# Optimization experiments

Measured on AMD Instinct MI355X. Metric: run time of the kernel, lower is better.

The kernel has to match this reference:

```python
import jax, jax.numpy as jnp
import numpy as np
from jax import lax

H = 256          # hidden_size
VOCAB = 30000
N_OPS = 9
N_COLS = 16
T = 4            # num_time_steps
Q = 64           # question length
N_NUM = 8        # numbers appearing in the question
ROWS = 1_000_000

# operation indices (Neural Programmer, ICLR 2016 op set)
OP_SUM, OP_COUNT, OP_DIFF, OP_GREATER, OP_LESSER, OP_AND, OP_OR, OP_ASSIGN, OP_RESET = range(N_OPS)


def setup_inputs() -> dict:
    key = jax.random.key(0)
    ks = jax.random.split(key, 13)
    s = 0.05
    f32 = jnp.float32
    return {
        "input_question": jax.random.randint(ks[0], (Q,), 0, VOCAB),
        "input_question_numbers": jax.random.randint(ks[1], (N_NUM,), 0, 100),
        "left_word_indices": jax.random.randint(ks[2], (N_NUM,), 0, Q),
        "table": jax.random.normal(ks[3], (ROWS, N_COLS), f32),
        # learned parameters
        "emb": jax.random.normal(ks[4], (VOCAB, H), f32) * s,      # question word embeddings
        "Wx": jax.random.normal(ks[5], (H, H), f32) * s,           # question RNN input weight
        "Wh": jax.random.normal(ks[6], (H, H), f32) * s,           # question RNN recurrent weight
        "W_op": jax.random.normal(ks[7], (H, 2 * H), f32) * s,     # selector (op branch)
        "op_emb": jax.random.normal(ks[8], (N_OPS, H), f32) * s,   # operation embeddings
        "W_col": jax.random.normal(ks[9], (H, 2 * H), f32) * s,    # selector (column branch)
        "col_emb": jax.random.normal(ks[10], (N_COLS, H), f32) * s,# column embeddings
        "W_hist": jax.random.normal(ks[11], (H, 3 * H), f32) * s,  # history RNN
        "U": jax.random.normal(ks[12], (2, H), f32) * s,           # lesser/greater pivot vectors
    }


def reference(input_question, input_question_numbers, left_word_indices, table,
              emb, Wx, Wh, W_op, op_emb, W_col, col_emb, W_hist, U):
    dt = table.dtype
    hid = Wx.shape[0]

    # ---- question RNN (simple tanh RNN) ----
    xs = emb[input_question]                               # [Q, H]
    def step(h, x):
        h2 = jnp.tanh(x @ Wx.T + h @ Wh.T)
        return h2, h2
    q, hs = lax.scan(step, jnp.zeros((hid,), dt), xs)      # q=[H], hs=[Q,H]

    # ---- pivot computation (z_matrix = hidden states left of each number) ----
    z = hs[left_word_indices]                              # [N_NUM, H]
    nums = input_question_numbers.astype(dt)               # [N_NUM]
    l_pivot = jax.nn.softmax(z @ U[0]) @ nums              # scalar
    g_pivot = jax.nn.softmax(z @ U[1]) @ nums              # scalar

    # soft comparison maps (pivots are timestep-independent; compute once)
    sel_l = jax.nn.sigmoid(l_pivot - table)                # [R, C] ~ [table < l_pivot]
    sel_g = jax.nn.sigmoid(table - g_pivot)                # [R, C] ~ [table > g_pivot]

    h_hist = jnp.zeros((hid,), dt)
    scalars = [jnp.zeros((), dt)]
    rs_list = [jnp.ones((table.shape[0],), dt)]
    lookup = jnp.zeros(table.shape, dt)

    for _ in range(T):
        rs1 = rs_list[-1]
        rs2 = rs_list[max(0, len(rs_list) - 2)]
        s1 = scalars[-1]
        s3 = scalars[max(0, len(scalars) - 3)]

        # selector: soft op / column distributions from [question; history]
        qh = jnp.concatenate([q, h_hist])                  # [2H]
        a_op = jax.nn.softmax(op_emb @ jnp.tanh(W_op @ qh))    # [N_OPS]
        a_col = jax.nn.softmax(col_emb @ jnp.tanh(W_col @ qh)) # [N_COLS]

        # row select (soft mixture over ops)
        rs = (a_op[OP_GREATER] * (sel_g @ a_col)
              + a_op[OP_LESSER] * (sel_l @ a_col)
              + a_op[OP_AND] * jnp.minimum(rs1, rs2)
              + a_op[OP_OR] * jnp.maximum(rs1, rs2)
              + a_op[OP_RESET] * jnp.ones_like(rs1)
              + (a_op[OP_SUM] + a_op[OP_COUNT] + a_op[OP_DIFF] + a_op[OP_ASSIGN]) * rs1)

        # scalar answer
        scalar = (a_op[OP_SUM] * jnp.sum(rs1 @ table)
                  + a_op[OP_COUNT] * jnp.sum(rs1)
                  + a_op[OP_DIFF] * (s3 - s1))

        # lookup answer: assign op prints selected rows/columns
        lookup = a_op[OP_ASSIGN] * rs[:, None] * a_col[None, :]

        # history RNN
        c = jnp.concatenate([a_op @ op_emb, a_col @ col_emb, h_hist])  # [3H]
        h_hist = jnp.tanh(W_hist @ c)

        rs_list.append(rs)
        scalars.append(scalar)

    return scalars[-1], lookup
```

## Files before the change

### kernel.cpp

```cpp
#include <hip/hip_runtime.h>
#include <hip/hip_fp16.h>
#include <math.h>

#define HDIM   256
#define QLEN   64
#define NNUM   8
#define NOPS   9
#define NCOLS  16
#define TSTEPS 4


#define WS_LPIV 0
#define WS_GPIV 1
#define WS_ACOL 2
#define WS_AOP  66
#define WS_Q    112
#define WS_PQO  368
#define WS_PQC  624
#define WS_HS   880
#define WS_XP   2928
#define WS_AH   19312
#define WS_BH   21616
#define WS_WH16 25712
#define WS_M16  42096
#define WS_PART 140400
#define NBLK_C  2048

typedef _Float16 f16x8 __attribute__((ext_vector_type(8)));
typedef _Float16 f16x4 __attribute__((ext_vector_type(4)));
typedef float    f32x4 __attribute__((ext_vector_type(4)));

__device__ __forceinline__ float fast_tanh(float x) {
    return 1.0f - 2.0f / (__expf(2.0f * x) + 1.0f);
}

__global__ void precompute_kernel(const int* __restrict__ q,
                                  const float* __restrict__ emb,
                                  const float* __restrict__ Wx,
                                  const float* __restrict__ Wh,
                                  const float* __restrict__ W_op,
                                  const float* __restrict__ W_col,
                                  const float* __restrict__ W_hist,
                                  const float* __restrict__ op_emb,
                                  const float* __restrict__ col_emb,
                                  float* __restrict__ ws) {
    int gid = blockIdx.x * 256 + threadIdx.x;
    if (gid < QLEN * HDIM) {
        int t = gid >> 8, j = gid & 255;
        const float4* x4 = (const float4*)(emb + (size_t)q[t] * HDIM);
        const float4* w4 = (const float4*)(Wx + (size_t)j * HDIM);
        float s = 0.f;
        for (int k = 0; k < HDIM / 4; k++) {
            float4 a = x4[k], b = w4[k];
            s += a.x * b.x + a.y * b.y + a.z * b.z + a.w * b.w;
        }
        ws[WS_XP + t * HDIM + j] = s;
    } else if (gid < QLEN * HDIM + HDIM * NOPS) {
        int idx = gid - QLEN * HDIM;
        int j = idx / NOPS, o = idx % NOPS;
        const float4* w4 = (const float4*)(W_hist + (size_t)j * (3 * HDIM));
        const float4* e4 = (const float4*)(op_emb + (size_t)o * HDIM);
        float s = 0.f;
        for (int k = 0; k < HDIM / 4; k++) {
            float4 a = w4[k], b = e4[k];
            s += a.x * b.x + a.y * b.y + a.z * b.z + a.w * b.w;
        }
        ws[WS_AH + idx] = s;
    } else if (gid < QLEN * HDIM + HDIM * NOPS + HDIM * NCOLS) {
        int idx = gid - QLEN * HDIM - HDIM * NOPS;
        int j = idx / NCOLS, c = idx % NCOLS;
        const float4* w4 = (const float4*)(W_hist + (size_t)j * (3 * HDIM) + HDIM);
        const float4* e4 = (const float4*)(col_emb + (size_t)c * HDIM);
        float s = 0.f;
        for (int k = 0; k < HDIM / 4; k++) {
            float4 a = w4[k], b = e4[k];
            s += a.x * b.x + a.y * b.y + a.z * b.z + a.w * b.w;
        }
        ws[WS_BH + idx] = s;
    } else if (gid < 22784 + 16384) {
        int did = gid - 22784;
        int hidx = did * 2;
        int e = hidx & 7, qr = (hidx >> 3) & 15, quad = (hidx >> 7) & 3;
        int kk = (hidx >> 9) & 7, w = hidx >> 12;
        const float* src = Wh + (size_t)(16 * w + qr) * HDIM + kk * 32 + quad * 8 + e;
        float2 v = *(const float2*)src;
        ((__half2*)(ws + WS_WH16))[did] = __floats2half2_rn(v.x, v.y);
    } else if (gid < 22784 + 16384 + 98304) {
        int did = gid - (22784 + 16384);
        int mat = did >> 15;
        int hidx = (did & 32767) * 2;
        int e = hidx & 7, j = (hidx >> 3) & 255, i = hidx >> 11;
        const float* src;
        if (mat == 0)      src = W_op   + (size_t)j * (2 * HDIM) + HDIM     + i * 8 + e;
        else if (mat == 1) src = W_col  + (size_t)j * (2 * HDIM) + HDIM     + i * 8 + e;
        else               src = W_hist + (size_t)j * (3 * HDIM) + 2 * HDIM + i * 8 + e;
        float2 v = *(const float2*)src;
        ((__half2*)(ws + WS_M16))[did] = __floats2half2_rn(v.x, v.y);
    }
}

__global__ __launch_bounds__(256, 1) void rnn_kernel(
        float* __restrict__ ws,
        const int* __restrict__ lwi) {
    __shared__ float xpL[QLEN * HDIM];
    __shared__ _Float16 hF[2][HDIM];
    __shared__ float preact[HDIM];
    __shared__ float hsL[NNUM * HDIM];
    __shared__ float hQ[HDIM];
    __shared__ unsigned stepmask[QLEN];

    const int tid = threadIdx.x;
    const int wave = tid >> 6, lane = tid & 63;
    const int quad = lane >> 4, qr = lane & 15;

    #pragma unroll
    for (int i = 0; i < 16; i++) {
        int idx = (i * 256 + tid) * 4;
        *(float4*)(xpL + idx) = *(const float4*)(ws + WS_XP + idx);
    }
    if (tid < QLEN) {
        unsigned m = 0;
        #pragma unroll
        for (int i = 0; i < NNUM; i++) m |= (lwi[i] == tid) ? (1u << i) : 0u;
        stepmask[tid] = m;
    }
    const _Float16* wsh = (const _Float16*)(ws + WS_WH16);
    f16x8 aW[4][8];
    #pragma unroll
    for (int r = 0; r < 4; r++)
        #pragma unroll
        for (int kk = 0; kk < 8; kk++)
            aW[r][kk] = *(const f16x8*)(wsh + ((size_t)(((4 * wave + r) * 8 + kk) * 64 + lane)) * 8);
    hF[0][tid] = (_Float16)0.f;
    __syncthreads();

    for (int s = 0; s < QLEN; s++) {
        #pragma unroll
        for (int r = 0; r < 4; r++)
            #pragma unroll
            for (int kk = 0; kk < 8; kk++) {
                f32x4 t = __builtin_bit_cast(f32x4, aW[r][kk]);
                asm volatile("" : "+v"(t));
                aW[r][kk] = __builtin_bit_cast(f16x8, t);
            }

        const _Float16* hb = hF[s & 1];
        f16x8 bfrag[8];
        #pragma unroll
        for (int kk = 0; kk < 8; kk++)
            bfrag[kk] = *(const f16x8*)(hb + kk * 32 + quad * 8);
        f32x4 acc[4];
        #pragma unroll
        for (int r = 0; r < 4; r++) acc[r] = (f32x4){0.f, 0.f, 0.f, 0.f};
        #pragma unroll
        for (int kk = 0; kk < 8; kk++)
            #pragma unroll
            for (int r = 0; r < 4; r++)
                acc[r] = __builtin_amdgcn_mfma_f32_16x16x32_f16(aW[r][kk], bfrag[kk], acc[r], 0, 0, 0);
        if (qr == 0) {
            #pragma unroll
            for (int r = 0; r < 4; r++) {
                int rb = 64 * wave + 16 * r + quad * 4;
                *(f32x4*)(preact + rb) = acc[r];
            }
        }
        __syncthreads();
        {
            float h = fast_tanh(preact[tid] + xpL[s * HDIM + tid]);
            hF[(s + 1) & 1][tid] = (_Float16)h;
            unsigned m = stepmask[s];
            while (m) {
                int i = __builtin_ctz(m);
                hsL[i * HDIM + tid] = h;
                m &= m - 1;
            }
            if (s == QLEN - 1) hQ[tid] = h;
        }
        __syncthreads();
    }
    #pragma unroll
    for (int i = 0; i < NNUM; i++) ws[WS_HS + i * HDIM + tid] = hsL[i * HDIM + tid];
    ws[WS_Q + tid] = hQ[tid];
}

__global__ void qproj_kernel(const float* __restrict__ W_op,
                             const float* __restrict__ W_col,
                             float* __restrict__ ws) {
    int gid = blockIdx.x * 256 + threadIdx.x;
    int dot = gid >> 5, l = gid & 31;
    int mat = dot >> 8, j = dot & 255;
    const float* w = (mat ? W_col : W_op) + (size_t)j * (2 * HDIM) + l * 8;
    const float* qv = ws + WS_Q + l * 8;
    float4 a0 = *(const float4*)w,        a1 = *(const float4*)(w + 4);
    float4 b0 = *(const float4*)qv,       b1 = *(const float4*)(qv + 4);
    float s = a0.x * b0.x + a0.y * b0.y + a0.z * b0.z + a0.w * b0.w
            + a1.x * b1.x + a1.y * b1.y + a1.z * b1.z + a1.w * b1.w;
    s += __shfl_xor(s, 1); s += __shfl_xor(s, 2); s += __shfl_xor(s, 4);
    s += __shfl_xor(s, 8); s += __shfl_xor(s, 16);
    if (l == 0) ws[(mat ? WS_PQC : WS_PQO) + j] = s;
}

__global__ __launch_bounds__(256) void select_kernel(
        float* __restrict__ ws,
        const float* __restrict__ U,
        const int* __restrict__ nums,
        const float* __restrict__ op_emb,
        const float* __restrict__ col_emb) {
    __shared__ float zu[16];
    __shared__ float hH[HDIM];
    __shared__ float top_op[HDIM], top_col[HDIM], mh[HDIM];
    __shared__ float logits[32];
    __shared__ float aop_s[NOPS], acol_s[NCOLS];

    const int tid = threadIdx.x;

    {
        int g = tid >> 4, l = tid & 15;
        int i = g >> 1, u = g & 1;
        const float* z = ws + WS_HS + i * HDIM + l * 16;
        const float* uu = U + u * HDIM + l * 16;
        float s = 0.f;
        #pragma unroll
        for (int k = 0; k < 4; k++) {
            float4 a = *(const float4*)(z + k * 4), b = *(const float4*)(uu + k * 4);
            s += a.x * b.x + a.y * b.y + a.z * b.z + a.w * b.w;
        }
        s += __shfl_xor(s, 1); s += __shfl_xor(s, 2);
        s += __shfl_xor(s, 4); s += __shfl_xor(s, 8);
        if (l == 0) zu[g] = s;
    }
    if (tid < HDIM) hH[tid] = 0.f;
    __syncthreads();
    if (tid == 0) {
        #pragma unroll
        for (int u = 0; u < 2; u++) {
            float mx = -1e30f;
            for (int i = 0; i < NNUM; i++) mx = fmaxf(mx, zu[i * 2 + u]);
            float se = 0.f, pv = 0.f;
            for (int i = 0; i < NNUM; i++) {
                float e = __expf(zu[i * 2 + u] - mx);
                se += e;
                pv += e * (float)nums[i];
            }
            ws[u] = pv / se;
        }
    }
    __syncthreads();

    const _Float16* wsm = (const _Float16*)(ws + WS_M16);
    const float pqo = ws[WS_PQO + tid];
    const float pqc = ws[WS_PQC + tid];

    for (int t = 0; t < TSTEPS; t++) {
        float so = 0.f, sc = 0.f, sh = 0.f;
        #pragma unroll
        for (int i = 0; i < 32; i++) {
            float4 h0 = *(const float4*)(hH + i * 8);
            float4 h1 = *(const float4*)(hH + i * 8 + 4);
            f16x8 a = *(const f16x8*)(wsm + ((size_t)(0 * 32 + i) * 256 + tid) * 8);
            f16x8 b = *(const f16x8*)(wsm + ((size_t)(1 * 32 + i) * 256 + tid) * 8);
            f16x8 c = *(const f16x8*)(wsm + ((size_t)(2 * 32 + i) * 256 + tid) * 8);
            so += (float)a[0]*h0.x + (float)a[1]*h0.y + (float)a[2]*h0.z + (float)a[3]*h0.w
                + (float)a[4]*h1.x + (float)a[5]*h1.y + (float)a[6]*h1.z + (float)a[7]*h1.w;
            sc += (float)b[0]*h0.x + (float)b[1]*h0.y + (float)b[2]*h0.z + (float)b[3]*h0.w
                + (float)b[4]*h1.x + (float)b[5]*h1.y + (float)b[6]*h1.z + (float)b[7]*h1.w;
            sh += (float)c[0]*h0.x + (float)c[1]*h0.y + (float)c[2]*h0.z + (float)c[3]*h0.w
                + (float)c[4]*h1.x + (float)c[5]*h1.y + (float)c[6]*h1.z + (float)c[7]*h1.w;
        }
        top_op[tid]  = fast_tanh(pqo + so);
        top_col[tid] = fast_tanh(pqc + sc);
        mh[tid] = sh;
        __syncthreads();

        #pragma unroll
        for (int d0 = 0; d0 < 32; d0 += 8) {
            int d = d0 + (tid >> 5), l = tid & 31;
            if (d < 25) {
                float s = 0.f;
                if (d < NOPS) {
                    const float* e = op_emb + (size_t)d * HDIM;
                    #pragma unroll
                    for (int m = 0; m < 8; m++) s += e[l * 8 + m] * top_op[l * 8 + m];
                } else {
                    const float* e = col_emb + (size_t)(d - NOPS) * HDIM;
                    #pragma unroll
                    for (int m = 0; m < 8; m++) s += e[l * 8 + m] * top_col[l * 8 + m];
                }
                s += __shfl_xor(s, 1); s += __shfl_xor(s, 2); s += __shfl_xor(s, 4);
                s += __shfl_xor(s, 8); s += __shfl_xor(s, 16);
                if (l == 0) logits[d] = s;
            }
        }
        __syncthreads();
        if (tid == 0) {
            float mx = -1e30f;
            for (int o = 0; o < NOPS; o++) mx = fmaxf(mx, logits[o]);
            float se = 0.f, e[NOPS];
            for (int o = 0; o < NOPS; o++) { e[o] = __expf(logits[o] - mx); se += e[o]; }
            for (int o = 0; o < NOPS; o++) {
                float a = e[o] / se;
                aop_s[o] = a;
                ws[WS_AOP + t * NOPS + o] = a;
            }
        } else if (tid == 32) {
            float mx = -1e30f;
            for (int c = 0; c < NCOLS; c++) mx = fmaxf(mx, logits[NOPS + c]);
            float se = 0.f, e[NCOLS];
            for (int c = 0; c < NCOLS; c++) { e[c] = __expf(logits[NOPS + c] - mx); se += e[c]; }
            for (int c = 0; c < NCOLS; c++) {
                float a = e[c] / se;
                acol_s[c] = a;
                ws[WS_ACOL + t * NCOLS + c] = a;
            }
        }
        __syncthreads();
        {
            float s = mh[tid];
            const float* ah = ws + WS_AH + tid * NOPS;
            #pragma unroll
            for (int o = 0; o < NOPS; o++) s += ah[o] * aop_s[o];
            const float* bh = ws + WS_BH + tid * NCOLS;
            #pragma unroll
            for (int c = 0; c < NCOLS; c++) s += bh[c] * acol_s[c];
            float hv = fast_tanh(s);
            __syncthreads();
            hH[tid] = hv;
        }
        __syncthreads();
    }
}

__global__ __launch_bounds__(256) void table_kernel(
        const float* __restrict__ table,
        const float* __restrict__ wsc,
        float* __restrict__ wspart,
        float* __restrict__ out,
        int rows) {
    const int tid = threadIdx.x;
    const int cq = tid & 3;
    const float lpiv = wsc[WS_LPIV];
    const float gpiv = wsc[WS_GPIV];
    float4 acol4[TSTEPS];
    float wg[TSTEPS], wl[TSTEPS], wand[TSTEPS], wor[TSTEPS], wrst[TSTEPS], wpass[TSTEPS];
    #pragma unroll
    for (int t = 0; t < TSTEPS; t++) {
        acol4[t] = make_float4(wsc[WS_ACOL + t * NCOLS + cq * 4 + 0],
                               wsc[WS_ACOL + t * NCOLS + cq * 4 + 1],
                               wsc[WS_ACOL + t * NCOLS + cq * 4 + 2],
                               wsc[WS_ACOL + t * NCOLS + cq * 4 + 3]);
        wg[t]   = wsc[WS_AOP + t * NOPS + 3];
        wl[t]   = wsc[WS_AOP + t * NOPS + 4];
        wand[t] = wsc[WS_AOP + t * NOPS + 5];
        wor[t]  = wsc[WS_AOP + t * NOPS + 6];
        wrst[t] = wsc[WS_AOP + t * NOPS + 8];
        wpass[t] = wsc[WS_AOP + t * NOPS + 0] + wsc[WS_AOP + t * NOPS + 1]
                 + wsc[WS_AOP + t * NOPS + 2] + wsc[WS_AOP + t * NOPS + 7];
    }
    const float wassign = wsc[WS_AOP + 3 * NOPS + 7];

    float dAcc[TSTEPS] = {0.f, 0.f, 0.f, 0.f};
    float nAcc[TSTEPS] = {0.f, 0.f, 0.f, 0.f};
    const long rowsL = rows;

    for (long r0 = (long)blockIdx.x * 64; r0 < rowsL; r0 += (long)NBLK_C * 64) {
        long row = r0 + (tid >> 2);
        bool valid = row < rowsL;
        f32x4 tv = {0.f, 0.f, 0.f, 0.f};
        if (valid)
            tv = __builtin_nontemporal_load((const f32x4*)(table + row * NCOLS + cq * 4));
        float prs = tv.x + tv.y + tv.z + tv.w;
        float pg[4], pl[4];
        {
            float c0 = tv.x, c1 = tv.y, c2 = tv.z, c3 = tv.w;
            float sg0 = __builtin_amdgcn_rcpf(1.f + __expf(gpiv - c0));
            float sg1 = __builtin_amdgcn_rcpf(1.f + __expf(gpiv - c1));
            float sg2 = __builtin_amdgcn_rcpf(1.f + __expf(gpiv - c2));
            float sg3 = __builtin_amdgcn_rcpf(1.f + __expf(gpiv - c3));
            float sl0 = __builtin_amdgcn_rcpf(1.f + __expf(c0 - lpiv));
            float sl1 = __builtin_amdgcn_rcpf(1.f + __expf(c1 - lpiv));
            float sl2 = __builtin_amdgcn_rcpf(1.f + __expf(c2 - lpiv));
            float sl3 = __builtin_amdgcn_rcpf(1.f + __expf(c3 - lpiv));
            #pragma unroll
            for (int t = 0; t < TSTEPS; t++) {
                pg[t] = sg0 * acol4[t].x + sg1 * acol4[t].y + sg2 * acol4[t].z + sg3 * acol4[t].w;
                pl[t] = sl0 * acol4[t].x + sl1 * acol4[t].y + sl2 * acol4[t].z + sl3 * acol4[t].w;
            }
        }
        prs += __shfl_xor(prs, 1); prs += __shfl_xor(prs, 2);
        #pragma unroll
        for (int t = 0; t < TSTEPS; t++) {
            pg[t] += __shfl_xor(pg[t], 1); pg[t] += __shfl_xor(pg[t], 2);
            pl[t] += __shfl_xor(pl[t], 1); pl[t] += __shfl_xor(pl[t], 2);
        }
        float rs1 = 1.f, rs2 = 1.f;
        float vf = valid ? 1.f : 0.f;
        #pragma unroll
        for (int i = 0; i < TSTEPS; i++) {
            dAcc[i] += vf * rs1 * prs;
            nAcc[i] += vf * rs1;
            float nrs = wg[i] * pg[i] + wl[i] * pl[i]
                      + wand[i] * fminf(rs1, rs2) + wor[i] * fmaxf(rs1, rs2)
                      + wrst[i] + wpass[i] * rs1;
            rs2 = rs1;
            rs1 = nrs;
        }
        if (valid) {
            float wa = wassign * rs1;
            float* ob = out + 1 + row * NCOLS + cq * 4;
            __builtin_nontemporal_store(wa * acol4[3].x, ob + 0);
            __builtin_nontemporal_store(wa * acol4[3].y, ob + 1);
            __builtin_nontemporal_store(wa * acol4[3].z, ob + 2);
            __builtin_nontemporal_store(wa * acol4[3].w, ob + 3);
        }
    }

    #pragma unroll
    for (int i = 0; i < TSTEPS; i++) {
        #pragma unroll
        for (int off = 32; off >= 1; off >>= 1) {
            dAcc[i] += __shfl_xor(dAcc[i], off);
            nAcc[i] += __shfl_xor(nAcc[i], off);
        }
    }
    __shared__ float redl[4][8];
    int wv = tid >> 6, ln = tid & 63;
    if (ln == 0) {
        #pragma unroll
        for (int i = 0; i < TSTEPS; i++) {
            redl[wv][i] = dAcc[i];
            redl[wv][4 + i] = nAcc[i];
        }
    }
    __syncthreads();
    if (tid < 8) {
        float s = redl[0][tid] + redl[1][tid] + redl[2][tid] + redl[3][tid];
        wspart[blockIdx.x * 8 + tid] = 0.25f * s;
    }
}

__global__ void finalize_kernel(const float* __restrict__ ws, float* __restrict__ out) {
    __shared__ float red[8];
    int a = threadIdx.x >> 5, l = threadIdx.x & 31;
    float s = 0.f;
    for (int b = l; b < NBLK_C; b += 32) s += ws[WS_PART + b * 8 + a];
    s += __shfl_xor(s, 1, 32); s += __shfl_xor(s, 2, 32); s += __shfl_xor(s, 4, 32);
    s += __shfl_xor(s, 8, 32); s += __shfl_xor(s, 16, 32);
    if (l == 0) red[a] = s;
    __syncthreads();
    if (threadIdx.x == 0) {
        float Dv[4] = {red[0], red[1], red[2], red[3]};
        float Nv[4] = {red[4], red[5], red[6], red[7]};
        const float* aop = ws + WS_AOP;
        float sc[5];
        sc[0] = 0.f;
        #pragma unroll
        for (int i = 0; i < 4; i++) {
            float s1 = sc[i];
            float s3 = sc[(i >= 2) ? (i - 2) : 0];
            sc[i + 1] = aop[i * NOPS + 0] * Dv[i] + aop[i * NOPS + 1] * Nv[i]
                      + aop[i * NOPS + 2] * (s3 - s1);
        }
        out[0] = sc[4];
    }
}

extern "C" void kernel_launch(void* const* d_in, const int* in_sizes, int n_in,
                              void* d_out, int out_size, void* d_ws, size_t ws_size,
                              hipStream_t stream) {
    const int*   q       = (const int*)d_in[0];
    const int*   nums    = (const int*)d_in[1];
    const int*   lwi     = (const int*)d_in[2];
    const float* table   = (const float*)d_in[3];
    const float* emb     = (const float*)d_in[4];
    const float* Wx      = (const float*)d_in[5];
    const float* Wh      = (const float*)d_in[6];
    const float* W_op    = (const float*)d_in[7];
    const float* op_emb  = (const float*)d_in[8];
    const float* W_col   = (const float*)d_in[9];
    const float* col_emb = (const float*)d_in[10];
    const float* W_hist  = (const float*)d_in[11];
    const float* U       = (const float*)d_in[12];
    float* out = (float*)d_out;
    float* ws  = (float*)d_ws;
    int rows = in_sizes[3] / NCOLS;

    const int pre_outputs = 137472;
    precompute_kernel<<<(pre_outputs + 255) / 256, 256, 0, stream>>>(
        q, emb, Wx, Wh, W_op, W_col, W_hist, op_emb, col_emb, ws);
    rnn_kernel<<<1, 256, 0, stream>>>(ws, lwi);
    qproj_kernel<<<64, 256, 0, stream>>>(W_op, W_col, ws);
    select_kernel<<<1, 256, 0, stream>>>(ws, U, nums, op_emb, col_emb);
    table_kernel<<<NBLK_C, 256, 0, stream>>>(
        table, ws, ws + WS_PART, out, rows);
    finalize_kernel<<<1, 256, 0, stream>>>(ws, out);
}
```

Baseline: 274.8 us.

## Overlap head-weight precompute with the serial question RNN via extra blocks

Moves the W_hist·op_emb and W_hist·col_emb projections and the fp16 repacking of the W_op/W_col/W_hist tails out of the precompute kernel. They now run in extra blocks of the RNN launch, so that work overlaps the single-block sequential recurrence instead of preceding it. The precompute kernel now converts all of Wh to fp16, and the fp16 workspace offsets are shifted to fit. The register-pinning asm barrier on the Wh fragments is hoisted out of the 64-step loop. The added blocks each reserve the RNN kernel's large shared-memory footprint, and the savings are bounded by how small the moved precompute work is.

```diff
diff --git a/kernel.cpp b/kernel.cpp
--- a/kernel.cpp
+++ b/kernel.cpp
@@ -22,8 +22,8 @@
 #define WS_AH   19312
 #define WS_BH   21616
 #define WS_WH16 25712
-#define WS_M16  42096
-#define WS_PART 140400
+#define WS_M16  58480
+#define WS_PART 156784
 #define NBLK_C  2048
 
 typedef _Float16 f16x8 __attribute__((ext_vector_type(8)));
@@ -38,11 +38,6 @@
                                   const float* __restrict__ emb,
                                   const float* __restrict__ Wx,
                                   const float* __restrict__ Wh,
-                                  const float* __restrict__ W_op,
-                                  const float* __restrict__ W_col,
-                                  const float* __restrict__ W_hist,
-                                  const float* __restrict__ op_emb,
-                                  const float* __restrict__ col_emb,
                                   float* __restrict__ ws) {
     int gid = blockIdx.x * 256 + threadIdx.x;
     if (gid < QLEN * HDIM) {
@@ -55,53 +50,63 @@
             s += a.x * b.x + a.y * b.y + a.z * b.z + a.w * b.w;
         }
         ws[WS_XP + t * HDIM + j] = s;
-    } else if (gid < QLEN * HDIM + HDIM * NOPS) {
-        int idx = gid - QLEN * HDIM;
-        int j = idx / NOPS, o = idx % NOPS;
-        const float4* w4 = (const float4*)(W_hist + (size_t)j * (3 * HDIM));
-        const float4* e4 = (const float4*)(op_emb + (size_t)o * HDIM);
-        float s = 0.f;
-        for (int k = 0; k < HDIM / 4; k++) {
-            float4 a = w4[k], b = e4[k];
-            s += a.x * b.x + a.y * b.y + a.z * b.z + a.w * b.w;
-        }
-        ws[WS_AH + idx] = s;
-    } else if (gid < QLEN * HDIM + HDIM * NOPS + HDIM * NCOLS) {
-        int idx = gid - QLEN * HDIM - HDIM * NOPS;
-        int j = idx / NCOLS, c = idx % NCOLS;
-        const float4* w4 = (const float4*)(W_hist + (size_t)j * (3 * HDIM) + HDIM);
-        const float4* e4 = (const float4*)(col_emb + (size_t)c * HDIM);
-        float s = 0.f;
-        for (int k = 0; k < HDIM / 4; k++) {
-            float4 a = w4[k], b = e4[k];
-            s += a.x * b.x + a.y * b.y + a.z * b.z + a.w * b.w;
-        }
-        ws[WS_BH + idx] = s;
-    } else if (gid < 22784 + 16384) {
-        int did = gid - 22784;
+    } else {
+        int did = gid - QLEN * HDIM;
         int hidx = did * 2;
         int e = hidx & 7, qr = (hidx >> 3) & 15, quad = (hidx >> 7) & 3;
-        int kk = (hidx >> 9) & 7, w = hidx >> 12;
-        const float* src = Wh + (size_t)(16 * w + qr) * HDIM + kk * 32 + quad * 8 + e;
+        int kk = (hidx >> 9) & 7, t = hidx >> 12;
+        const float* src = Wh + (size_t)(16 * t + qr) * HDIM + kk * 32 + quad * 8 + e;
         float2 v = *(const float2*)src;
         ((__half2*)(ws + WS_WH16))[did] = __floats2half2_rn(v.x, v.y);
-    } else if (gid < 22784 + 16384 + 98304) {
-        int did = gid - (22784 + 16384);
-        int mat = did >> 15;
-        int hidx = (did & 32767) * 2;
-        int e = hidx & 7, j = (hidx >> 3) & 255, i = hidx >> 11;
-        const float* src;
-        if (mat == 0)      src = W_op   + (size_t)j * (2 * HDIM) + HDIM     + i * 8 + e;
-        else if (mat == 1) src = W_col  + (size_t)j * (2 * HDIM) + HDIM     + i * 8 + e;
-        else               src = W_hist + (size_t)j * (3 * HDIM) + 2 * HDIM + i * 8 + e;
-        float2 v = *(const float2*)src;
-        ((__half2*)(ws + WS_M16))[did] = __floats2half2_rn(v.x, v.y);
     }
 }
 
 __global__ __launch_bounds__(256, 1) void rnn_kernel(
         float* __restrict__ ws,
-        const int* __restrict__ lwi) {
+        const int* __restrict__ lwi,
+        const float* __restrict__ W_op,
+        const float* __restrict__ W_col,
+        const float* __restrict__ W_hist,
+        const float* __restrict__ op_emb,
+        const float* __restrict__ col_emb) {
+    if (blockIdx.x != 0) {
+        int gid = (blockIdx.x - 1) * 256 + threadIdx.x;
+        if (gid < HDIM * NOPS) {
+            int j = gid / NOPS, o = gid % NOPS;
+            const float4* w4 = (const float4*)(W_hist + (size_t)j * (3 * HDIM));
+            const float4* e4 = (const float4*)(op_emb + (size_t)o * HDIM);
+            float s = 0.f;
+            for (int k = 0; k < HDIM / 4; k++) {
+                float4 a = w4[k], b = e4[k];
+                s += a.x * b.x + a.y * b.y + a.z * b.z + a.w * b.w;
+            }
+            ws[WS_AH + gid] = s;
+        } else if (gid < HDIM * NOPS + HDIM * NCOLS) {
+            int idx = gid - HDIM * NOPS;
+            int j = idx / NCOLS, c = idx % NCOLS;
+            const float4* w4 = (const float4*)(W_hist + (size_t)j * (3 * HDIM) + HDIM);
+            const float4* e4 = (const float4*)(col_emb + (size_t)c * HDIM);
+            float s = 0.f;
+            for (int k = 0; k < HDIM / 4; k++) {
+                float4 a = w4[k], b = e4[k];
+                s += a.x * b.x + a.y * b.y + a.z * b.z + a.w * b.w;
+            }
+            ws[WS_BH + idx] = s;
+        } else if (gid < HDIM * NOPS + HDIM * NCOLS + 98304) {
+            int did = gid - (HDIM * NOPS + HDIM * NCOLS);
+            int mat = did >> 15;
+            int hidx = (did & 32767) * 2;
+            int e = hidx & 7, j = (hidx >> 3) & 255, i = hidx >> 11;
+            const float* src;
+            if (mat == 0)      src = W_op   + (size_t)j * (2 * HDIM) + HDIM     + i * 8 + e;
+            else if (mat == 1) src = W_col  + (size_t)j * (2 * HDIM) + HDIM     + i * 8 + e;
+            else               src = W_hist + (size_t)j * (3 * HDIM) + 2 * HDIM + i * 8 + e;
+            float2 v = *(const float2*)src;
+            ((__half2*)(ws + WS_M16))[did] = __floats2half2_rn(v.x, v.y);
+        }
+        return;
+    }
+
     __shared__ float xpL[QLEN * HDIM];
     __shared__ _Float16 hF[2][HDIM];
     __shared__ float preact[HDIM];
@@ -131,19 +136,18 @@
         #pragma unroll
         for (int kk = 0; kk < 8; kk++)
             aW[r][kk] = *(const f16x8*)(wsh + ((size_t)(((4 * wave + r) * 8 + kk) * 64 + lane)) * 8);
+    #pragma unroll
+    for (int r = 0; r < 4; r++)
+        #pragma unroll
+        for (int kk = 0; kk < 8; kk++) {
+            f32x4 t = __builtin_bit_cast(f32x4, aW[r][kk]);
+            asm volatile("" : "+v"(t));
+            aW[r][kk] = __builtin_bit_cast(f16x8, t);
+        }
     hF[0][tid] = (_Float16)0.f;
     __syncthreads();
 
     for (int s = 0; s < QLEN; s++) {
-        #pragma unroll
-        for (int r = 0; r < 4; r++)
-            #pragma unroll
-            for (int kk = 0; kk < 8; kk++) {
-                f32x4 t = __builtin_bit_cast(f32x4, aW[r][kk]);
-                asm volatile("" : "+v"(t));
-                aW[r][kk] = __builtin_bit_cast(f16x8, t);
-            }
-
         const _Float16* hb = hF[s & 1];
         f16x8 bfrag[8];
         #pragma unroll
@@ -484,10 +488,10 @@
     float* ws  = (float*)d_ws;
     int rows = in_sizes[3] / NCOLS;
 
-    const int pre_outputs = 137472;
-    precompute_kernel<<<(pre_outputs + 255) / 256, 256, 0, stream>>>(
-        q, emb, Wx, Wh, W_op, W_col, W_hist, op_emb, col_emb, ws);
-    rnn_kernel<<<1, 256, 0, stream>>>(ws, lwi);
+    precompute_kernel<<<192, 256, 0, stream>>>(q, emb, Wx, Wh, ws);
+    const int pre2_threads = HDIM * NOPS + HDIM * NCOLS + 98304;
+    rnn_kernel<<<1 + (pre2_threads + 255) / 256, 256, 0, stream>>>(
+        ws, lwi, W_op, W_col, W_hist, op_emb, col_emb);
     qproj_kernel<<<64, 256, 0, stream>>>(W_op, W_col, ws);
     select_kernel<<<1, 256, 0, stream>>>(ws, U, nums, op_emb, col_emb);
     table_kernel<<<NBLK_C, 256, 0, stream>>>(
```

New measurement: 268.6 us. 1.02x faster.
